# Performance work log

Measured on AMD Instinct MI355X. Metric: run time of the kernel, lower is better.

The kernel has to match this reference:

```python
import jax, jax.numpy as jnp
import numpy as np

B, N, D = 8, 1024, 512
H, DH = 8, 64          # num_heads, dim_head_output
MLP = 2048
PRUNE_NUM = 64         # remove_num > 0 -> prune branch of determine_fuse
KEEP_NUM = 3
NEG = -1e10


def setup_inputs() -> dict:
    key = jax.random.key(0)
    ks = jax.random.split(key, 10)
    s = 0.02
    inp = {
        "x": jax.random.normal(ks[0], (B, N, D), dtype=jnp.float32),
        "mask": (jax.random.uniform(ks[1], (B, N, N)) < 0.1).astype(jnp.float32),
        "Wqkv": jax.random.normal(ks[2], (D, 3 * H * DH), dtype=jnp.float32) * s,
        "Wout": jax.random.normal(ks[3], (H * DH, D), dtype=jnp.float32) * s,
        "bout": jnp.zeros((D,), jnp.float32),
        "ln1_g": jnp.ones((D,), jnp.float32),
        "ln1_b": jnp.zeros((D,), jnp.float32),
        "ln2_g": jnp.ones((D,), jnp.float32),
        "ln2_b": jnp.zeros((D,), jnp.float32),
        "W1": jax.random.normal(ks[4], (D, MLP), dtype=jnp.float32) * s,
        "b1": jnp.zeros((MLP,), jnp.float32),
        "W2": jax.random.normal(ks[5], (MLP, D), dtype=jnp.float32) * s,
        "b2": jnp.zeros((D,), jnp.float32),
    }
    return inp


def _layer_norm(x, g, b, eps=1e-5):
    mu = jnp.mean(x, axis=-1, keepdims=True)
    var = jnp.mean((x - mu) ** 2, axis=-1, keepdims=True)
    return (x - mu) * jax.lax.rsqrt(var + eps) * g + b


def _attention_with_gos(h, mask, Wqkv, Wout, bout):
    # qkv projection (no bias), chunk into q,k,v then b n (h d) -> b h n d
    qkv = h @ Wqkv                                  # [B,N,3*H*DH]
    q, k, v = jnp.split(qkv, 3, axis=-1)
    def heads(t):
        return t.reshape(B, N, H, DH).transpose(0, 2, 1, 3)  # bhnd
    q, k, v = heads(q), heads(k), heads(v)
    scale = DH ** -0.5
    scores = jnp.einsum("bhnd,bhmd->bhnm", q, k) * scale
    scores = jnp.where(mask[:, None, :, :] == 1.0, NEG, scores)
    attw = jax.nn.softmax(scores, axis=-1)          # [B,H,N,N]
    out = jnp.einsum("bhnm,bhmd->bhnd", attw, v)
    out = out.transpose(0, 2, 1, 3).reshape(B, N, H * DH)
    out = out @ Wout + bout                         # [B,N,D] (dropout=0 -> identity)

    # att_weights_topk = attw.mean(heads)[:, 0]; [:,0] = -inf
    att_topk = attw.mean(axis=1)[:, 0]              # [B,N]
    att_topk = att_topk.at[:, 0].set(-jnp.inf)

    # determine_fuse (prune branch, remove_num > 0)
    nrm = jnp.linalg.norm(out, axis=2, keepdims=True)
    normed = out / jnp.maximum(nrm, 1e-12)          # F.normalize(p=2, dim=2)
    cos = jnp.einsum("bnd,bmd->bnm", normed, normed)
    idx = jnp.arange(N)
    cos = cos.at[:, idx, idx].set(-jnp.inf)
    cos = cos.at[:, 0, :].set(-jnp.inf)
    cos = cos.at[:, :, 0].set(-jnp.inf)
    # NOTE: torch also computes topk of cos.view(B,-1) with k=(N-1)^2, but the
    # result is unused in the remove_num>0 branch (dead code under jit).

    # torch.topk(att_topk, N) sorted descending -> argsort of -att_topk
    attentive_idx = jnp.argsort(-att_topk, axis=1)  # [B,N]
    # pruned = attentive_idx[:, :N-1][:, -PRUNE_NUM:]
    what_to_prune = attentive_idx[:, N - 1 - PRUNE_NUM : N - 1]
    what_to_merge = jnp.full((B, 1), -1, dtype=jnp.int32)
    survived_mask = jnp.zeros((B, 1 + KEEP_NUM, 1 + KEEP_NUM), dtype=jnp.int32)
    return out, what_to_prune, what_to_merge, survived_mask


def reference(x, mask, Wqkv, Wout, bout, ln1_g, ln1_b, ln2_g, ln2_b, W1, b1, W2, b2):
    h = _layer_norm(x, ln1_g, ln1_b)
    att_out, what_to_prune, what_to_merge, survived_mask = _attention_with_gos(
        h, mask, Wqkv, Wout, bout)
    x = x + att_out
    h2 = _layer_norm(x, ln2_g, ln2_b)
    ff = jax.nn.gelu(h2 @ W1 + b1, approximate=False) @ W2 + b2
    x = x + ff
    return x, what_to_prune, what_to_merge, survived_mask
```

## Files before the change

kernel.cpp:

```cpp
#include <hip/hip_runtime.h>
#include <hip/hip_bf16.h>
#include <math.h>

#define BB 8
#define NN 1024
#define DD 512
#define HH 8
#define DHH 64
#define MLPD 2048

typedef __attribute__((ext_vector_type(8))) short short8;
typedef __attribute__((ext_vector_type(4))) float f32x4;

#define MFMA16(a,b,c) __builtin_amdgcn_mfma_f32_16x16x32_bf16(a,b,c,0,0,0)

#define QSCALE 0.18033688011112042f
#define NEGBIG 0xCE6E6B28u

__device__ __forceinline__ short f2bf(float f) {
  union { float f; unsigned u; } x; x.f = f;
  unsigned r = x.u + 0x7FFFu + ((x.u >> 16) & 1u);
  return (short)(r >> 16);
}

__device__ __forceinline__ void gl_lds16(const short* g, short* l) {
  __builtin_amdgcn_global_load_lds(
      (const __attribute__((address_space(1))) unsigned int*)g,
      (__attribute__((address_space(3))) unsigned int*)l, 16, 0, 0);
}

__device__ __forceinline__ float gelu_fast(float t) {
  const float u = 0.7978845608028654f * (t + 0.044715f * t * t * t);
  const float e = __builtin_amdgcn_exp2f(u * 2.8853900817779268f);
  return t - t * __builtin_amdgcn_rcpf(e + 1.0f);
}

template<bool WF32>
__global__ __launch_bounds__(256) void ln_kernel(const float* __restrict__ x,
    const float* __restrict__ gam, const float* __restrict__ bet,
    short* __restrict__ ob, float* __restrict__ of)
{
  const int row = blockIdx.x;
  const int tid = threadIdx.x;
  const float2 xv = *(const float2*)(x + (size_t)row*DD + tid*2);
  double s = (double)xv.x + (double)xv.y;
  for (int o = 32; o >= 1; o >>= 1) s += __shfl_down(s, o, 64);
  __shared__ double red[4];
  const int l = tid & 63, w = tid >> 6;
  if (l == 0) red[w] = s;
  __syncthreads();
  const double mu = (red[0]+red[1]+red[2]+red[3]) * (1.0/512.0);
  const double d0 = (double)xv.x - mu, d1 = (double)xv.y - mu;
  double q = d0*d0 + d1*d1;
  for (int o = 32; o >= 1; o >>= 1) q += __shfl_down(q, o, 64);
  __syncthreads();
  if (l == 0) red[w] = q;
  __syncthreads();
  const double var = (red[0]+red[1]+red[2]+red[3]) * (1.0/512.0);
  const float rs = (float)(1.0 / sqrt(var + 1e-5));
  const float mf = (float)mu;
  const float y0 = (xv.x - mf)*rs*gam[tid*2]   + bet[tid*2];
  const float y1 = (xv.y - mf)*rs*gam[tid*2+1] + bet[tid*2+1];
  ob[(size_t)row*DD + tid*2]   = f2bf(y0);
  ob[(size_t)row*DD + tid*2+1] = f2bf(y1);
  if (WF32) {
    of[(size_t)row*DD + tid*2]   = y0;
    of[(size_t)row*DD + tid*2+1] = y1;
  }
}

__global__ __launch_bounds__(256) void wt_kernel(const float* __restrict__ W,
    short* __restrict__ Wt, int K, int N)
{
  __shared__ float tile[32][33];
  const int n0 = blockIdx.x * 32, k0 = blockIdx.y * 32;
  const int tx = threadIdx.x & 31, ty = threadIdx.x >> 5;
  #pragma unroll
  for (int j = 0; j < 4; j++)
    tile[ty + j*8][tx] = W[(size_t)(k0 + ty + j*8)*N + n0 + tx];
  __syncthreads();
  #pragma unroll
  for (int j = 0; j < 4; j++)
    Wt[(size_t)(n0 + ty + j*8)*K + k0 + tx] = f2bf(tile[tx][ty + j*8]);
}

__global__ __launch_bounds__(256) void maskpack_kernel(const float* __restrict__ mask,
    unsigned long long* __restrict__ mb)
{
  const int wid = blockIdx.x*256 + threadIdx.x;
  if (wid >= BB*NN*16) return;
  const int r = wid >> 4, c = wid & 15;
  const float4* p = (const float4*)(mask + (size_t)r*NN + c*64);
  unsigned long long m = 0;
  #pragma unroll
  for (int i = 0; i < 16; i++) {
    const float4 v = p[i];
    unsigned long long mm = 0;
    if (v.x == 1.0f) mm |= 1ULL;
    if (v.y == 1.0f) mm |= 2ULL;
    if (v.z == 1.0f) mm |= 4ULL;
    if (v.w == 1.0f) mm |= 8ULL;
    m |= mm << (i*4);
  }
  mb[wid] = m;
}

template<int BN, int EPI, int NBUF>
__global__ __launch_bounds__(256) void gemm_bt(
    const short* __restrict__ A, const short* __restrict__ Bt,
    int M, int N, int K,
    const float* __restrict__ bias, const float* __restrict__ res,
    float* __restrict__ outf, short* __restrict__ outb,
    short* __restrict__ outQ, short* __restrict__ outK, short* __restrict__ outVt)
{
  constexpr int CH = 8 + BN/16;
  constexpr int L  = CH/4;
  constexpr int BUFS = (128 + BN)*32;
  __shared__ __align__(16) short lds[NBUF*BUFS];
  const int tid = threadIdx.x;
  const int bm0 = blockIdx.x * 128;
  const int bn0 = blockIdx.y * BN;
  const int lane = tid & 63, wid = tid >> 6;
  const int wm = (wid >> 1) * 64, wn = (wid & 1) * (BN/2);
  const int lr = lane & 15, lg = lane >> 4;
  constexpr int NT = BN/32;

  const short* gsrc[L];
  int loff[L];
  const int scc = (((lane & 3) ^ ((lane >> 3) & 3)))*8;
  #pragma unroll
  for (int i = 0; i < L; i++) {
    const int c = i*4 + wid;
    const int rr = ((c < 8) ? c : c - 8)*16 + (lane >> 2);
    gsrc[i] = (c < 8) ? (A + (size_t)(bm0 + rr)*K + scc)
                      : (Bt + (size_t)(bn0 + rr)*K + scc);
    loff[i] = c*512;
  }
  const int xs = (lr >> 1) & 3;

  f32x4 acc[4][NT];
  #pragma unroll
  for (int i = 0; i < 4; i++)
    #pragma unroll
    for (int j = 0; j < NT; j++) acc[i][j] = f32x4{0.f,0.f,0.f,0.f};

  const int nsteps = K >> 5;

  auto STAGE = [&](int buf, int t) {
    short* dst = lds + buf*BUFS;
    const int ko = t*32;
    #pragma unroll
    for (int i = 0; i < L; i++)
      gl_lds16(gsrc[i] + ko, dst + loff[i]);
  };
  auto COMPUTE = [&](const short* bufA) {
    const short* bufB = bufA + 4096;
    short8 af[4], bfr[NT];
    #pragma unroll
    for (int mt = 0; mt < 4; mt++)
      af[mt] = *(const short8*)(bufA + (wm + mt*16 + lr)*32 + (lg ^ xs)*8);
    #pragma unroll
    for (int nt = 0; nt < NT; nt++)
      bfr[nt] = *(const short8*)(bufB + (wn + nt*16 + lr)*32 + (lg ^ xs)*8);
    __builtin_amdgcn_s_setprio(1);
    #pragma unroll
    for (int mt = 0; mt < 4; mt++)
      #pragma unroll
      for (int nt = 0; nt < NT; nt++)
        acc[mt][nt] = MFMA16(af[mt], bfr[nt], acc[mt][nt]);
    __builtin_amdgcn_s_setprio(0);
  };

  if constexpr (NBUF == 2) {
    STAGE(0, 0);
    asm volatile("s_waitcnt vmcnt(0)" ::: "memory");
    __builtin_amdgcn_s_barrier();
    int cur = 0;
    #pragma unroll 1
    for (int t = 0; t < nsteps; t++) {
      if (t + 1 < nsteps) STAGE(cur ^ 1, t + 1);
      COMPUTE(lds + cur*BUFS);
      asm volatile("s_waitcnt vmcnt(0)" ::: "memory");
      __builtin_amdgcn_s_barrier();
      cur ^= 1;
    }
  } else {
    STAGE(0, 0);
    STAGE(1, 1);
    int cur = 0;
    #pragma unroll 1
    for (int t = 0; t < nsteps; t++) {
      if (t == nsteps - 1) {
        asm volatile("s_waitcnt vmcnt(0)" ::: "memory");
      } else if constexpr (L == 4) {
        asm volatile("s_waitcnt vmcnt(4)" ::: "memory");
      } else {
        asm volatile("s_waitcnt vmcnt(3)" ::: "memory");
      }
      __builtin_amdgcn_s_barrier();
      if (t + 2 < nsteps) {
        const int bnext = (cur == 0) ? 2 : cur - 1;
        STAGE(bnext, t + 2);
      }
      COMPUTE(lds + cur*BUFS);
      cur = (cur == 2) ? 0 : cur + 1;
    }
  }

  if (EPI == 0 && bn0 >= 1024) {
    #pragma unroll
    for (int mt = 0; mt < 4; mt++)
      #pragma unroll
      for (int nt = 0; nt < NT; nt++) {
        const int row0 = bm0 + wm + mt*16 + lg*4;
        const int b = row0 >> 10, tok0 = row0 & 1023;
        const int c2 = bn0 + wn + nt*16 + lr - 1024;
        const int h = c2 >> 6, d = c2 & 63;
        unsigned lo2, hi2;
        asm("v_cvt_pk_bf16_f32 %0, %1, %2" : "=v"(lo2)
            : "v"(acc[mt][nt][0]), "v"(acc[mt][nt][1]));
        asm("v_cvt_pk_bf16_f32 %0, %1, %2" : "=v"(hi2)
            : "v"(acc[mt][nt][2]), "v"(acc[mt][nt][3]));
        uint2 pw; pw.x = lo2; pw.y = hi2;
        *(uint2*)(outVt + (((size_t)(b*HH + h))*DHH + d)*NN + tok0) = pw;
      }
    return;
  }

  #pragma unroll
  for (int mt = 0; mt < 4; mt++)
    #pragma unroll
    for (int nt = 0; nt < NT; nt++)
      #pragma unroll
      for (int r = 0; r < 4; r++) {
        const int row = bm0 + wm + mt*16 + lg*4 + r;
        const int col = bn0 + wn + nt*16 + lr;
        const float v = acc[mt][nt][r];
        if (EPI == 0) {
          const int b = row >> 10, tok = row & 1023;
          if (col < 512) {
            const int h = col >> 6, d = col & 63;
            outQ[(((size_t)(b*HH + h))*NN + tok)*DHH + d] = f2bf(v * QSCALE);
          } else {
            const int c2 = col - 512, h = c2 >> 6, d = c2 & 63;
            outK[(((size_t)(b*HH + h))*NN + tok)*DHH + d] = f2bf(v);
          }
        } else if (EPI == 1) {
          outf[(size_t)row*N + col] = v + bias[col] + res[(size_t)row*N + col];
        } else {
          outb[(size_t)row*N + col] = f2bf(gelu_fast(v + bias[col]));
        }
      }
}

__global__ __launch_bounds__(256) void attn_kernel(
    const short* __restrict__ Qg, const short* __restrict__ Kg,
    const short* __restrict__ Vtg, const unsigned long long* __restrict__ mb,
    short* __restrict__ attout)
{
  const int qb = blockIdx.x;
  const int bh = blockIdx.y;
  const int b = bh >> 3, h = bh & 7;
  const int tid = threadIdx.x, lane = tid & 63, w = tid >> 6;
  const int lr = lane & 15, lg = lane >> 4;

  __shared__ __align__(16) short K0[64*72], K1[64*72];
  __shared__ __align__(16) short V0[64*72], V1[64*72];
  __shared__ __align__(16) short PsA[4][16*72], PsB[4][16*72];

  const int qA = qb*128 + w*32 + lr;
  const int qB = qA + 16;
  short* PsAw = &PsA[w][0];
  short* PsBw = &PsB[w][0];

  const size_t qbase = (size_t)bh*NN*DHH;
  const short8 bqA0 = *(const short8*)(Qg + qbase + (size_t)qA*DHH + lg*8);
  const short8 bqA1 = *(const short8*)(Qg + qbase + (size_t)qA*DHH + 32 + lg*8);
  const short8 bqB0 = *(const short8*)(Qg + qbase + (size_t)qB*DHH + lg*8);
  const short8 bqB1 = *(const short8*)(Qg + qbase + (size_t)qB*DHH + 32 + lg*8);

  const unsigned long long* mrowA = mb + ((size_t)b*NN + qA)*16;
  const unsigned long long* mrowB = mb + ((size_t)b*NN + qB)*16;

  const int sidx0 = tid, sidx1 = tid + 256;
  const int doff0 = (sidx0>>3)*72 + (sidx0&7)*8;
  const int doff1 = (sidx1>>3)*72 + (sidx1&7)*8;
  auto kgp = [&](int kc, int idx) {
    return Kg + ((size_t)bh*NN + kc*64 + (idx>>3))*DHH + (idx&7)*8;
  };
  auto vgp = [&](int kc, int idx) {
    return Vtg + ((size_t)bh*DHH + (idx>>3))*NN + kc*64 + (idx&7)*8;
  };

  uint4 kr0, kr1, vr0, vr1;
  unsigned long long mAc, mBc, mAn, mBn;

  kr0 = *(const uint4*)kgp(0, sidx0); kr1 = *(const uint4*)kgp(0, sidx1);
  vr0 = *(const uint4*)vgp(0, sidx0); vr1 = *(const uint4*)vgp(0, sidx1);
  mAc = mrowA[0]; mBc = mrowB[0];
  *(uint4*)(K0 + doff0) = kr0; *(uint4*)(K0 + doff1) = kr1;
  *(uint4*)(V0 + doff0) = vr0; *(uint4*)(V0 + doff1) = vr1;
  __syncthreads();

  f32x4 oA[4], oB[4];
  #pragma unroll
  for (int dt = 0; dt < 4; dt++) { oA[dt] = f32x4{0.f,0.f,0.f,0.f}; oB[dt] = f32x4{0.f,0.f,0.f,0.f}; }
  float lsumA = 0.f, lsumB = 0.f;

#define ATT_BODY(CK, CV, NK, NV, MAc, MBc, MAn, MBn, KC, LAST)                 \
  {                                                                            \
    if (!(LAST)) {                                                             \
      kr0 = *(const uint4*)kgp((KC)+1, sidx0);                                 \
      kr1 = *(const uint4*)kgp((KC)+1, sidx1);                                 \
      vr0 = *(const uint4*)vgp((KC)+1, sidx0);                                 \
      vr1 = *(const uint4*)vgp((KC)+1, sidx1);                                 \
      MAn = mrowA[(KC)+1]; MBn = mrowB[(KC)+1];                                \
    }                                                                          \
                              \
    f32x4 sA[4], sB[4];                                                        \
    {                                                                          \
      const unsigned long long mqA = MAc >> (lg*4);                            \
      const unsigned loA = (unsigned)mqA, hiA = (unsigned)(mqA >> 32);         \
      const unsigned long long mqB = MBc >> (lg*4);                            \
      const unsigned loB = (unsigned)mqB, hiB = (unsigned)(mqB >> 32);         \
      _Pragma("unroll")                                                        \
      for (int nt = 0; nt < 4; nt++) {                                         \
        const unsigned wA = (nt < 2) ? loA : hiA;                              \
        const unsigned wB = (nt < 2) ? loB : hiB;                              \
        const int sh = (nt & 1) * 16;                                          \
        _Pragma("unroll")                                                      \
        for (int rr = 0; rr < 4; rr++) {                                       \
          const unsigned bA = (wA >> (sh + rr)) & 1u;                          \
          const unsigned bB = (wB >> (sh + rr)) & 1u;                          \
          sA[nt][rr] = __uint_as_float((0u - bA) & NEGBIG);                    \
          sB[nt][rr] = __uint_as_float((0u - bB) & NEGBIG);                    \
        }                                                                      \
      }                                                                        \
    }                                                                          \
    __builtin_amdgcn_s_setprio(1);                                             \
    _Pragma("unroll")                                                          \
    for (int nt = 0; nt < 4; nt++) {                                           \
      const short8 ak0 = *(const short8*)((CK) + (nt*16 + lr)*72 + lg*8);      \
      const short8 ak1 = *(const short8*)((CK) + (nt*16 + lr)*72 + 32 + lg*8); \
      sA[nt] = MFMA16(ak0, bqA0, sA[nt]);                                      \
      sA[nt] = MFMA16(ak1, bqA1, sA[nt]);                                      \
      sB[nt] = MFMA16(ak0, bqB0, sB[nt]);                                      \
      sB[nt] = MFMA16(ak1, bqB1, sB[nt]);                                      \
    }                                                                          \
    __builtin_amdgcn_s_setprio(0);                                             \
    _Pragma("unroll")                                                          \
    for (int nt = 0; nt < 4; nt++) {                                           \
      const float a0 = __builtin_amdgcn_exp2f(sA[nt][0]);                      \
      const float a1 = __builtin_amdgcn_exp2f(sA[nt][1]);                      \
      const float a2 = __builtin_amdgcn_exp2f(sA[nt][2]);                      \
      const float a3 = __builtin_amdgcn_exp2f(sA[nt][3]);                      \
      lsumA += (a0 + a1) + (a2 + a3);                                          \
      unsigned plo, phi;                                                       \
      asm("v_cvt_pk_bf16_f32 %0, %1, %2" : "=v"(plo) : "v"(a0), "v"(a1));      \
      asm("v_cvt_pk_bf16_f32 %0, %1, %2" : "=v"(phi) : "v"(a2), "v"(a3));      \
      uint2 pw; pw.x = plo; pw.y = phi;                                        \
      *(uint2*)(PsAw + lr*72 + nt*16 + lg*4) = pw;                             \
      const float c0 = __builtin_amdgcn_exp2f(sB[nt][0]);                      \
      const float c1 = __builtin_amdgcn_exp2f(sB[nt][1]);                      \
      const float c2 = __builtin_amdgcn_exp2f(sB[nt][2]);                      \
      const float c3 = __builtin_amdgcn_exp2f(sB[nt][3]);                      \
      lsumB += (c0 + c1) + (c2 + c3);                                          \
      unsigned qlo, qhi;                                                       \
      asm("v_cvt_pk_bf16_f32 %0, %1, %2" : "=v"(qlo) : "v"(c0), "v"(c1));      \
      asm("v_cvt_pk_bf16_f32 %0, %1, %2" : "=v"(qhi) : "v"(c2), "v"(c3));      \
      uint2 qw; qw.x = qlo; qw.y = qhi;                                        \
      *(uint2*)(PsBw + lr*72 + nt*16 + lg*4) = qw;                             \
    }                                                                          \
    {                                                                          \
      const short8 bpA0 = *(const short8*)(PsAw + lr*72 + lg*8);               \
      const short8 bpA1 = *(const short8*)(PsAw + lr*72 + 32 + lg*8);          \
      const short8 bpB0 = *(const short8*)(PsBw + lr*72 + lg*8);               \
      const short8 bpB1 = *(const short8*)(PsBw + lr*72 + 32 + lg*8);          \
      __builtin_amdgcn_s_setprio(1);                                           \
      _Pragma("unroll")                                                        \
      for (int dt = 0; dt < 4; dt++) {                                         \
        const short8 av0 = *(const short8*)((CV) + (dt*16 + lr)*72 + lg*8);    \
        const short8 av1 = *(const short8*)((CV) + (dt*16 + lr)*72 + 32 + lg*8);\
        oA[dt] = MFMA16(av0, bpA0, oA[dt]);                                    \
        oA[dt] = MFMA16(av1, bpA1, oA[dt]);                                    \
        oB[dt] = MFMA16(av0, bpB0, oB[dt]);                                    \
        oB[dt] = MFMA16(av1, bpB1, oB[dt]);                                    \
      }                                                                        \
      __builtin_amdgcn_s_setprio(0);                                           \
    }                                                                          \
    if (!(LAST)) {                                                             \
      *(uint4*)((NK) + doff0) = kr0; *(uint4*)((NK) + doff1) = kr1;            \
      *(uint4*)((NV) + doff0) = vr0; *(uint4*)((NV) + doff1) = vr1;            \
      MAc = MAn; MBc = MBn;                                                    \
      __syncthreads();                                                         \
    }                                                                          \
  }

  #pragma unroll 1
  for (int kc = 0; kc < 16; kc += 2) {
    ATT_BODY(K0, V0, K1, V1, mAc, mBc, mAn, mBn, kc, false)
    ATT_BODY(K1, V1, K0, V0, mAc, mBc, mAn, mBn, kc+1, (kc+1) == 15)
  }
#undef ATT_BODY

  lsumA += __shfl_xor(lsumA, 16, 64);
  lsumA += __shfl_xor(lsumA, 32, 64);
  lsumB += __shfl_xor(lsumB, 16, 64);
  lsumB += __shfl_xor(lsumB, 32, 64);
  const float linvA = 1.0f / lsumA;
  const float linvB = 1.0f / lsumB;

  #pragma unroll
  for (int dt = 0; dt < 4; dt++) {
    unsigned w0, w1, w2, w3;
    const float a0 = oA[dt][0]*linvA, a1 = oA[dt][1]*linvA;
    const float a2 = oA[dt][2]*linvA, a3 = oA[dt][3]*linvA;
    asm("v_cvt_pk_bf16_f32 %0, %1, %2" : "=v"(w0) : "v"(a0), "v"(a1));
    asm("v_cvt_pk_bf16_f32 %0, %1, %2" : "=v"(w1) : "v"(a2), "v"(a3));
    uint2 ow; ow.x = w0; ow.y = w1;
    *(uint2*)(PsAw + lr*72 + dt*16 + lg*4) = ow;
    const float c0 = oB[dt][0]*linvB, c1 = oB[dt][1]*linvB;
    const float c2 = oB[dt][2]*linvB, c3 = oB[dt][3]*linvB;
    asm("v_cvt_pk_bf16_f32 %0, %1, %2" : "=v"(w2) : "v"(c0), "v"(c1));
    asm("v_cvt_pk_bf16_f32 %0, %1, %2" : "=v"(w3) : "v"(c2), "v"(c3));
    uint2 ow2; ow2.x = w2; ow2.y = w3;
    *(uint2*)(PsBw + lr*72 + dt*16 + lg*4) = ow2;
  }
  #pragma unroll
  for (int rep = 0; rep < 2; rep++) {
    const int c = lane + rep*64;
    const int row = c >> 3, off = c & 7;
    const uint4 ovA = *(const uint4*)(PsAw + row*72 + off*8);
    *(uint4*)(attout + ((size_t)b*NN + qb*128 + w*32 + row)*DD + h*DHH + off*8) = ovA;
    const uint4 ovB = *(const uint4*)(PsBw + row*72 + off*8);
    *(uint4*)(attout + ((size_t)b*NN + qb*128 + w*32 + 16 + row)*DD + h*DHH + off*8) = ovB;
  }
}

__global__ __launch_bounds__(512) void q0_kernel(const float* __restrict__ hlnf,
    const float* __restrict__ Wqkv, double* __restrict__ q0)
{
  const int bh = blockIdx.x, b = bh >> 3, h = bh & 7;
  const int d = threadIdx.x & 63, cg = threadIdx.x >> 6;
  double acc = 0.0;
  #pragma unroll 8
  for (int c = cg*64; c < cg*64 + 64; c++)
    acc += (double)hlnf[(size_t)b*NN*DD + c] * (double)Wqkv[(size_t)c*1536 + h*64 + d];
  __shared__ double red[512];
  red[threadIdx.x] = acc;
  __syncthreads();
  if (threadIdx.x < 64) {
    double s = 0.0;
    #pragma unroll
    for (int g = 0; g < 8; g++) s += red[g*64 + d];
    q0[bh*64 + d] = s;
  }
}

__global__ __launch_bounds__(512) void wv_kernel(const float* __restrict__ Wqkv,
    const double* __restrict__ q0, double* __restrict__ wv)
{
  const int bh = blockIdx.x, h = bh & 7;
  __shared__ double q0s[64];
  if (threadIdx.x < 64) q0s[threadIdx.x] = q0[bh*64 + threadIdx.x];
  __syncthreads();
  const int c = threadIdx.x;
  const float4* wp = (const float4*)(Wqkv + (size_t)c*1536 + 512 + h*64);
  double acc = 0.0;
  #pragma unroll
  for (int dv = 0; dv < 16; dv++) {
    const float4 wq = wp[dv];
    acc += q0s[dv*4+0]*(double)wq.x + q0s[dv*4+1]*(double)wq.y
         + q0s[dv*4+2]*(double)wq.z + q0s[dv*4+3]*(double)wq.w;
  }
  wv[(size_t)bh*512 + c] = acc;
}

__global__ __launch_bounds__(256) void srow_kernel(const float* __restrict__ hlnf,
    const double* __restrict__ wv, const float* __restrict__ mask,
    double* __restrict__ srow)
{
  const int b = blockIdx.x, jc = blockIdx.y;
  const int jl = threadIdx.x >> 3;
  const int cg = threadIdx.x & 7;
  const int j  = jc*32 + jl;
  __shared__ double lw[8*512];
  __shared__ double red[32][8][9];
  for (int i = threadIdx.x; i < 4096; i += 256) lw[i] = wv[(size_t)b*4096 + i];
  __syncthreads();
  double acc[8] = {0,0,0,0,0,0,0,0};
  const float* xr = hlnf + ((size_t)b*NN + j)*DD;
  #pragma unroll
  for (int i = 0; i < 16; i++) {
    const int c = cg*4 + i*32;
    const float4 xv4 = *(const float4*)(xr + c);
    #pragma unroll
    for (int h = 0; h < 8; h++) {
      const double* lwc = lw + h*512 + c;
      acc[h] += (double)xv4.x*lwc[0] + (double)xv4.y*lwc[1]
              + (double)xv4.z*lwc[2] + (double)xv4.w*lwc[3];
    }
  }
  #pragma unroll
  for (int h = 0; h < 8; h++) red[jl][cg][h] = acc[h];
  __syncthreads();
  const int j2 = threadIdx.x >> 3, h2 = threadIdx.x & 7;
  double s = 0.0;
  #pragma unroll
  for (int g = 0; g < 8; g++) s += red[j2][g][h2];
  s *= 0.125;
  const float mval = mask[(size_t)b*NN*NN + jc*32 + j2];
  if (mval == 1.0f) s = -1e10;
  srow[((size_t)b*8 + h2)*NN + jc*32 + j2] = s;
}

__global__ __launch_bounds__(256) void msum_kernel(const double* __restrict__ srow,
    double* __restrict__ ms)
{
  const int bh = blockIdx.x;
  const double* s = srow + (size_t)bh*NN;
  double mx = -1e300;
  for (int j = threadIdx.x; j < NN; j += 256) mx = fmax(mx, s[j]);
  for (int o = 32; o >= 1; o >>= 1) mx = fmax(mx, __shfl_xor(mx, o, 64));
  __shared__ double red[4];
  if ((threadIdx.x & 63) == 0) red[threadIdx.x >> 6] = mx;
  __syncthreads();
  mx = fmax(fmax(red[0], red[1]), fmax(red[2], red[3]));
  double sum = 0.0;
  for (int j = threadIdx.x; j < NN; j += 256) sum += exp(s[j] - mx);
  for (int o = 32; o >= 1; o >>= 1) sum += __shfl_xor(sum, o, 64);
  __syncthreads();
  if ((threadIdx.x & 63) == 0) red[threadIdx.x >> 6] = sum;
  __syncthreads();
  if (threadIdx.x == 0) { ms[bh*2] = mx; ms[bh*2+1] = red[0]+red[1]+red[2]+red[3]; }
}

__global__ __launch_bounds__(1024) void sort_kernel(const double* __restrict__ srow,
    const double* __restrict__ ms, float* __restrict__ dout,
    int offP, int offM, int offS)
{
  const int b = blockIdx.x;
  const int j = threadIdx.x;
  __shared__ double vals[1024];
  __shared__ int    idx[1024];
  double a;
  if (j == 0) a = -INFINITY;
  else {
    double t = 0.0;
    #pragma unroll
    for (int h = 0; h < 8; h++) {
      const double m  = ms[(b*8 + h)*2];
      const double su = ms[(b*8 + h)*2 + 1];
      t += exp(srow[((size_t)b*8 + h)*NN + j] - m) / su;
    }
    a = t * 0.125;
  }
  vals[j] = a; idx[j] = j;
  for (int k = 2; k <= 1024; k <<= 1)
    for (int jj = k >> 1; jj > 0; jj >>= 1) {
      __syncthreads();
      const int ixj = j ^ jj;
      if (ixj > j) {
        const double v1 = vals[j], v2 = vals[ixj];
        const int i1 = idx[j], i2 = idx[ixj];
        const bool less12 = (v1 > v2) || (v1 == v2 && i1 < i2);
        const bool up = ((j & k) == 0);
        if (up ? !less12 : less12) {
          vals[j] = v2; vals[ixj] = v1; idx[j] = i2; idx[ixj] = i1;
        }
      }
    }
  __syncthreads();
  if (j >= 959 && j <= 1022) dout[offP + b*64 + (j - 959)] = (float)idx[j];
  if (b == 0) {
    if (j < 8)   dout[offM + j] = -1.0f;
    if (j < 128) dout[offS + j] = 0.0f;
  }
}

extern "C" void kernel_launch(void* const* d_in, const int* in_sizes, int n_in,
                              void* d_out, int out_size, void* d_ws, size_t ws_size,
                              hipStream_t stream) {
  (void)in_sizes; (void)n_in; (void)out_size; (void)ws_size;
  const float* x     = (const float*)d_in[0];
  const float* mask  = (const float*)d_in[1];
  const float* Wqkv  = (const float*)d_in[2];
  const float* Wout  = (const float*)d_in[3];
  const float* bout  = (const float*)d_in[4];
  const float* ln1g  = (const float*)d_in[5];
  const float* ln1b  = (const float*)d_in[6];
  const float* ln2g  = (const float*)d_in[7];
  const float* ln2b  = (const float*)d_in[8];
  const float* W1    = (const float*)d_in[9];
  const float* b1    = (const float*)d_in[10];
  const float* W2    = (const float*)d_in[11];
  const float* b2    = (const float*)d_in[12];
  float* dout = (float*)d_out;

  const size_t MB = 1ull << 20;
  char* ws = (char*)d_ws;
  short*  hln_bf = (short*)(ws + 0);
  float*  hlnf   = (float*)(ws + 8*MB);
  short*  Qg     = (short*)(ws + 24*MB);
  short*  Kg     = (short*)(ws + 32*MB);
  short*  Vtg    = (short*)(ws + 40*MB);
  unsigned long long* mbits = (unsigned long long*)(ws + 48*MB);
  short*  Wqkvt  = (short*)(ws + 49*MB);
  short*  Woutt  = (short*)(ws + 51*MB);
  short*  W1t    = (short*)(ws + 52*MB);
  short*  W2t    = (short*)(ws + 54*MB);
  double* q0v    = (double*)(ws + 56*MB);
  double* wvv    = (double*)(ws + 56*MB + 256*1024);
  double* srow   = (double*)(ws + 57*MB);
  double* msv    = (double*)(ws + 58*MB);
  short*  attout = (short*)(ws + 60*MB);
  float*  x1     = (float*)(ws + 68*MB);
  short*  h2     = (short*)(ws + 84*MB);
  short*  gbuf   = (short*)(ws + 0);

  const int offP = BB*NN*DD;
  const int offM = offP + BB*64;
  const int offS = offM + BB;

  ln_kernel<true><<<BB*NN, 256, 0, stream>>>(x, ln1g, ln1b, hln_bf, hlnf);

  q0_kernel<<<BB*HH, 512, 0, stream>>>(hlnf, Wqkv, q0v);
  wv_kernel<<<BB*HH, 512, 0, stream>>>(Wqkv, q0v, wvv);
  srow_kernel<<<dim3(BB, 32), 256, 0, stream>>>(hlnf, wvv, mask, srow);
  msum_kernel<<<BB*HH, 256, 0, stream>>>(srow, msv);
  sort_kernel<<<BB, 1024, 0, stream>>>(srow, msv, dout, offP, offM, offS);

  maskpack_kernel<<<(BB*NN*16)/256, 256, 0, stream>>>(mask, mbits);
  wt_kernel<<<dim3(1536/32, 512/32),  256, 0, stream>>>(Wqkv, Wqkvt, 512, 1536);
  wt_kernel<<<dim3(512/32, 512/32),   256, 0, stream>>>(Wout, Woutt, 512, 512);
  wt_kernel<<<dim3(2048/32, 512/32),  256, 0, stream>>>(W1,   W1t,   512, 2048);
  wt_kernel<<<dim3(512/32, 2048/32),  256, 0, stream>>>(W2,   W2t,   2048, 512);

  gemm_bt<128,0,3><<<dim3(64, 12), 256, 0, stream>>>(hln_bf, Wqkvt, BB*NN, 1536, 512,
      nullptr, nullptr, nullptr, nullptr, Qg, Kg, Vtg);

  attn_kernel<<<dim3(8, 64), 256, 0, stream>>>(Qg, Kg, Vtg, mbits, attout);

  gemm_bt<64,1,3><<<dim3(64, 8), 256, 0, stream>>>(attout, Woutt, BB*NN, 512, 512,
      bout, x, x1, nullptr, nullptr, nullptr, nullptr);

  ln_kernel<false><<<BB*NN, 256, 0, stream>>>(x1, ln2g, ln2b, h2, nullptr);

  gemm_bt<128,2,2><<<dim3(64, 16), 256, 0, stream>>>(h2, W1t, BB*NN, 2048, 512,
      b1, nullptr, nullptr, gbuf, nullptr, nullptr, nullptr);

  gemm_bt<64,1,3><<<dim3(64, 8), 256, 0, stream>>>(gbuf, W2t, BB*NN, 512, 2048,
      b2, x1, dout, nullptr, nullptr, nullptr, nullptr);
}
```

Measured before the change: 214.6 us.

## Stage attention K/V tiles via direct global-to-LDS loads with XOR swizzle

```diff
diff --git a/kernel.cpp b/kernel.cpp
--- a/kernel.cpp
+++ b/kernel.cpp
@@ -258,14 +258,15 @@
     const short* __restrict__ Vtg, const unsigned long long* __restrict__ mb,
     short* __restrict__ attout)
 {
-  const int qb = blockIdx.x;
-  const int bh = blockIdx.y;
+  const int id = blockIdx.x;
+  const int bh = (id & 7)*8 + ((id >> 3) & 7);
+  const int qb = id >> 6;
   const int b = bh >> 3, h = bh & 7;
   const int tid = threadIdx.x, lane = tid & 63, w = tid >> 6;
   const int lr = lane & 15, lg = lane >> 4;
 
-  __shared__ __align__(16) short K0[64*72], K1[64*72];
-  __shared__ __align__(16) short V0[64*72], V1[64*72];
+  __shared__ __align__(16) short K0[64*64], K1[64*64];
+  __shared__ __align__(16) short V0[64*64], V1[64*64];
   __shared__ __align__(16) short PsA[4][16*72], PsB[4][16*72];
 
   const int qA = qb*128 + w*32 + lr;
@@ -282,25 +283,27 @@
   const unsigned long long* mrowA = mb + ((size_t)b*NN + qA)*16;
   const unsigned long long* mrowB = mb + ((size_t)b*NN + qB)*16;
 
-  const int sidx0 = tid, sidx1 = tid + 256;
-  const int doff0 = (sidx0>>3)*72 + (sidx0&7)*8;
-  const int doff1 = (sidx1>>3)*72 + (sidx1&7)*8;
-  auto kgp = [&](int kc, int idx) {
-    return Kg + ((size_t)bh*NN + kc*64 + (idx>>3))*DHH + (idx&7)*8;
+  const int l8 = lane >> 3;
+  const int uu = (lane & 7) ^ l8;
+  const short* kgA = Kg + ((size_t)bh*NN + w*16 + l8)*64 + uu*8;
+  const short* kgB = kgA + 8*64;
+  const short* vgA = Vtg + ((size_t)bh*DHH + w*16 + l8)*NN + uu*8;
+  const short* vgB = vgA + 8*NN;
+  auto STAGE = [&](short* kb, short* vb, int kc) {
+    gl_lds16(kgA + kc*4096, kb + (w*16)*64);
+    gl_lds16(kgB + kc*4096, kb + (w*16 + 8)*64);
+    gl_lds16(vgA + kc*64,   vb + (w*16)*64);
+    gl_lds16(vgB + kc*64,   vb + (w*16 + 8)*64);
   };
-  auto vgp = [&](int kc, int idx) {
-    return Vtg + ((size_t)bh*DHH + (idx>>3))*NN + kc*64 + (idx&7)*8;
-  };
-
-  uint4 kr0, kr1, vr0, vr1;
+  const int xo0 = ((lg ^ (lr & 7)))*8;
+  const int xo1 = (((lg ^ (lr & 7))) ^ 4)*8;
+
   unsigned long long mAc, mBc, mAn, mBn;
 
-  kr0 = *(const uint4*)kgp(0, sidx0); kr1 = *(const uint4*)kgp(0, sidx1);
-  vr0 = *(const uint4*)vgp(0, sidx0); vr1 = *(const uint4*)vgp(0, sidx1);
+  STAGE(K0, V0, 0);
   mAc = mrowA[0]; mBc = mrowB[0];
-  *(uint4*)(K0 + doff0) = kr0; *(uint4*)(K0 + doff1) = kr1;
-  *(uint4*)(V0 + doff0) = vr0; *(uint4*)(V0 + doff1) = vr1;
-  __syncthreads();
+  asm volatile("s_waitcnt vmcnt(0)" ::: "memory");
+  __builtin_amdgcn_s_barrier();
 
   f32x4 oA[4], oB[4];
   #pragma unroll
@@ -310,10 +313,7 @@
 #define ATT_BODY(CK, CV, NK, NV, MAc, MBc, MAn, MBn, KC, LAST)                 \
   {                                                                            \
     if (!(LAST)) {                                                             \
-      kr0 = *(const uint4*)kgp((KC)+1, sidx0);                                 \
-      kr1 = *(const uint4*)kgp((KC)+1, sidx1);                                 \
-      vr0 = *(const uint4*)vgp((KC)+1, sidx0);                                 \
-      vr1 = *(const uint4*)vgp((KC)+1, sidx1);                                 \
+      STAGE(NK, NV, (KC)+1);                                                   \
       MAn = mrowA[(KC)+1]; MBn = mrowB[(KC)+1];                                \
     }                                                                          \
                               \
@@ -340,8 +340,9 @@
     __builtin_amdgcn_s_setprio(1);                                             \
     _Pragma("unroll")                                                          \
     for (int nt = 0; nt < 4; nt++) {                                           \
-      const short8 ak0 = *(const short8*)((CK) + (nt*16 + lr)*72 + lg*8);      \
-      const short8 ak1 = *(const short8*)((CK) + (nt*16 + lr)*72 + 32 + lg*8); \
+      const short* kr = (CK) + (nt*16 + lr)*64;                                \
+      const short8 ak0 = *(const short8*)(kr + xo0);                           \
+      const short8 ak1 = *(const short8*)(kr + xo1);                           \
       sA[nt] = MFMA16(ak0, bqA0, sA[nt]);                                      \
       sA[nt] = MFMA16(ak1, bqA1, sA[nt]);                                      \
       sB[nt] = MFMA16(ak0, bqB0, sB[nt]);                                      \
@@ -379,8 +380,9 @@
       __builtin_amdgcn_s_setprio(1);                                           \
       _Pragma("unroll")                                                        \
       for (int dt = 0; dt < 4; dt++) {                                         \
-        const short8 av0 = *(const short8*)((CV) + (dt*16 + lr)*72 + lg*8);    \
-        const short8 av1 = *(const short8*)((CV) + (dt*16 + lr)*72 + 32 + lg*8);\
+        const short* vr = (CV) + (dt*16 + lr)*64;                              \
+        const short8 av0 = *(const short8*)(vr + xo0);                         \
+        const short8 av1 = *(const short8*)(vr + xo1);                         \
         oA[dt] = MFMA16(av0, bpA0, oA[dt]);                                    \
         oA[dt] = MFMA16(av1, bpA1, oA[dt]);                                    \
         oB[dt] = MFMA16(av0, bpB0, oB[dt]);                                    \
@@ -389,10 +391,9 @@
       __builtin_amdgcn_s_setprio(0);                                           \
     }                                                                          \
     if (!(LAST)) {                                                             \
-      *(uint4*)((NK) + doff0) = kr0; *(uint4*)((NK) + doff1) = kr1;            \
-      *(uint4*)((NV) + doff0) = vr0; *(uint4*)((NV) + doff1) = vr1;            \
+      asm volatile("s_waitcnt vmcnt(0)" ::: "memory");                         \
+      __builtin_amdgcn_s_barrier();                                            \
       MAc = MAn; MBc = MBn;                                                    \
-      __syncthreads();                                                         \
     }                                                                          \
   }
 
@@ -639,7 +640,7 @@
   gemm_bt<128,0,3><<<dim3(64, 12), 256, 0, stream>>>(hln_bf, Wqkvt, BB*NN, 1536, 512,
       nullptr, nullptr, nullptr, nullptr, Qg, Kg, Vtg);
 
-  attn_kernel<<<dim3(8, 64), 256, 0, stream>>>(Qg, Kg, Vtg, mbits, attout);
+  attn_kernel<<<512, 256, 0, stream>>>(Qg, Kg, Vtg, mbits, attout);
 
   gemm_bt<64,1,3><<<dim3(64, 8), 256, 0, stream>>>(attout, Woutt, BB*NN, 512, 512,
       bout, x, x1, nullptr, nullptr, nullptr, nullptr);
```

Measured after the change: 212.2 us. Within noise of the previous version (-1.1%).
